# Performance work log

Measured on AMD Instinct MI355X. Metric: run time of the kernel, lower is better.

Reference implementation:

```python
import jax, jax.numpy as jnp
import numpy as np

EMBED_DIM = 512
SE_HIDDEN = max(1, int(EMBED_DIM * 0.25))  # 128
LN_EPS = 1e-5


def setup_inputs() -> dict:
    key = jax.random.key(0)
    ks = jax.random.split(key, 16)
    B, H, W, D = 8, 32, 32, EMBED_DIM
    s = 0.02
    return {
        "q": jax.random.normal(ks[0], (B, H, W, D), jnp.float32),
        "k": jax.random.normal(ks[1], (B, H, W, D), jnp.float32),
        "v": jax.random.normal(ks[2], (B, H, W, D), jnp.float32),
        # Linear weights stored as [in, out] (equivalent to torch W.T)
        "Wq": jax.random.normal(ks[3], (D, D), jnp.float32) * s,
        "Wk": jax.random.normal(ks[4], (D, D), jnp.float32) * s,
        "Wv": jax.random.normal(ks[5], (D, D), jnp.float32) * s,
        "Wo": jax.random.normal(ks[6], (D, D), jnp.float32) * s,
        # Conv2d kernel in HWIO layout for NHWC conv
        "conv_w": jax.random.normal(ks[7], (3, 3, D, D), jnp.float32) * s,
        "conv_b": jnp.zeros((D,), jnp.float32),
        "se_w1": jax.random.normal(ks[8], (D, SE_HIDDEN), jnp.float32) * s,
        "se_b1": jnp.zeros((SE_HIDDEN,), jnp.float32),
        "se_w2": jax.random.normal(ks[9], (SE_HIDDEN, D), jnp.float32) * s,
        "se_b2": jnp.zeros((D,), jnp.float32),
        "ln_g": jnp.ones((D,), jnp.float32),
        "ln_b": jnp.zeros((D,), jnp.float32),
    }


def _layernorm(x, g, b):
    mu = jnp.mean(x, axis=-1, keepdims=True)
    var = jnp.mean(jnp.square(x - mu), axis=-1, keepdims=True)
    return (x - mu) * jax.lax.rsqrt(var + LN_EPS) * g + b


def reference(q, k, v, Wq, Wk, Wv, Wo, conv_w, conv_b,
              se_w1, se_b1, se_w2, se_b2, ln_g, ln_b):
    B, H, W, D = q.shape
    scaler = jnp.sqrt(jnp.asarray(D, q.dtype))
    qp = q @ Wq  # [B,H,W,D]
    kp = k @ Wk
    vp = v @ Wv
    N = H * W
    qf = qp.reshape(B, N, D)
    kf = kp.reshape(B, N, D)
    vf = vp.reshape(B, N, D)
    scores = jnp.einsum('bnd,bmd->bnm', qf, kf) / scaler
    probs = jax.nn.softmax(scores, axis=-1)  # dropout p=0 -> identity
    out = jnp.einsum('bnm,bmd->bnd', probs, vf).reshape(B, H, W, D)
    out = out @ Wo
    # 3x3 same conv in NHWC
    out = jax.lax.conv_general_dilated(
        out, conv_w, window_strides=(1, 1), padding='SAME',
        dimension_numbers=('NHWC', 'HWIO', 'NHWC')) + conv_b
    # squeeze-excite: global average pool over spatial dims
    se = jnp.mean(out, axis=(1, 2))  # [B,D]
    se = jax.nn.silu(se @ se_w1 + se_b1)
    se = jax.nn.sigmoid(se @ se_w2 + se_b2)  # [B,D]
    out = out * se[:, None, None, :]
    x = qp + out  # residual uses q AFTER q_proj (q reassigned in torch code)
    return _layernorm(x, ln_g, ln_b)
```

## Files before the change

kernel.cpp:

```cpp
#include <hip/hip_runtime.h>
#include <hip/hip_bf16.h>

using bf16 = __hip_bfloat16;
typedef __attribute__((ext_vector_type(8))) short short8;
typedef __attribute__((ext_vector_type(4))) float f32x4;

static const size_t OFF_QP   = 0;
static const size_t OFF_KP   = (size_t)8  << 20;
static const size_t OFF_VPT  = (size_t)16 << 20;
static const size_t OFF_SC   = (size_t)24 << 20;
static const size_t OFF_PA   = (size_t)40 << 20;
static const size_t OFF_WT   = (size_t)56 << 20;
static const size_t OFF_CWT  = (size_t)58 << 20;
static const size_t OFF_POOL = (size_t)63 << 20;
static const size_t OFF_SE   = ((size_t)63 << 20) + 16384;
static const size_t OFF_RS   = ((size_t)63 << 20) + 32768;

__global__ __launch_bounds__(256) void prep_k(const float* __restrict__ Wq,
                                              const float* __restrict__ Wk,
                                              const float* __restrict__ Wv,
                                              const float* __restrict__ Wo,
                                              const float* __restrict__ convw,
                                              bf16* __restrict__ wT,
                                              bf16* __restrict__ cwT,
                                              float* __restrict__ pooled) {
    long idx = (long)blockIdx.x * 256 + threadIdx.x;
    if (idx < 4l * 262144) {
        int m = (int)(idx >> 18);
        int o = (int)(idx & 262143);
        int n = o >> 9, k = o & 511;
        const float* W = (m == 0) ? Wq : (m == 1) ? Wk : (m == 2) ? Wv : Wo;
        wT[idx] = __float2bfloat16(W[k * 512 + n]);
    } else if (idx < 4l * 262144 + 512l * 4608) {
        long o = idx - 4l * 262144;
        int co = (int)(o / 4608), t = (int)(o % 4608);
        cwT[o] = __float2bfloat16(convw[(long)t * 512 + co]);
    } else if (idx < 4l * 262144 + 512l * 4608 + 4096) {
        pooled[idx - (4l * 262144 + 512l * 4608)] = 0.f;
    }
}

__device__ __forceinline__ float bf2f(unsigned short h) {
    union { unsigned int u; float f; } c;
    c.u = (unsigned int)h << 16;
    return c.f;
}

template <int OP>
__global__ __launch_bounds__(256, 2) void gemm_k(
    const void* __restrict__ Ap0, const void* __restrict__ Ap1, const void* __restrict__ Ap2,
    int lda, long sA,
    const bf16* __restrict__ BT, int ldb, long sB,
    void* __restrict__ Cp, int ldc, long sC,
    int K, const float* __restrict__ bias, float* __restrict__ pooled,
    float* __restrict__ rs) {
    __shared__ bf16 As[2][128 * 64];
    __shared__ bf16 Bs[2][128 * 64];
    const int tid = threadIdx.x;
    const int l = tid & 63, w = tid >> 6;
    const int wm = w >> 1, wn = w & 1;

    const int gx = gridDim.x, gy = gridDim.y;
    const int nwg = gx * gy * gridDim.z;
    const int bid = blockIdx.x + gx * (blockIdx.y + gy * blockIdx.z);
    const int swz = (bid & 7) * (nwg >> 3) + (bid >> 3);
    const int bx = swz % gx;
    const int rem = swz / gx;
    const int by = rem % gy;
    const int zb = rem / gy;

    const int m0 = by * 128, n0 = bx * 128;
    const float isc = 0.04419417382415922f;

    int kbase = 0;
    const bf16* Ab = nullptr;
    const float* Af = nullptr;
    const bf16* Bb = BT;
    if (OP == 1) {
        Af = (const float*)(zb == 0 ? Ap0 : zb == 1 ? Ap1 : Ap2);
        Bb = BT + (long)zb * 262144;
    } else if (OP == 2) {
        Ab = (const bf16*)Ap0 + (long)zb * sA;
        Bb = BT + (long)zb * sB;
    } else if (OP == 3) {
        Ab = (const bf16*)Ap0;
        kbase = zb * 2304;
    } else if (OP == 4) {
        Ab = (const bf16*)Ap0 + (long)(zb & 7) * sA;
        Bb = BT + (long)(zb & 7) * sB;
        kbase = (zb >> 3) * 512;
    } else {
        Ab = (const bf16*)Ap0;
    }

    const int fr = l & 15;
    f32x4 acc[4][4] = {};
    float esum[4] = {0.f, 0.f, 0.f, 0.f};

    int pixoff[4], hh_[4], wp_[4];
    if (OP == 3) {
#pragma unroll
        for (int i = 0; i < 4; ++i) {
            int s = tid + i * 256;
            int row = s >> 3, c = s & 7;
            int p = m0 + row;
            int bb = p >> 10;
            hh_[i] = (p >> 5) & 31;
            wp_[i] = p & 31;
            pixoff[i] = ((bb * 32 + hh_[i]) * 32 + wp_[i]) * 512 + c * 8;
        }
    }
    float rinv_[4];
    if (OP == 5) {
#pragma unroll
        for (int i = 0; i < 4; ++i) {
            int row = m0 + ((tid + i * 256) >> 3);
            rinv_[i] = 1.0f / (rs[row] + rs[8192 + row]);
        }
    }

    short8 ar[4];
    float4 af0[4], af1[4];
    short8 br[4];

    auto stage_load = [&](int t) {
        int k0 = kbase + t * 64;
        int dy = 0, dx = 0, doff = 0;
        if (OP == 3) {
            int tap = k0 >> 9;
            dy = tap / 3 - 1;
            dx = tap % 3 - 1;
            doff = (dy * 32 + dx) * 512 + (k0 & 511);
        }
#pragma unroll
        for (int i = 0; i < 4; ++i) {
            int s = tid + i * 256;
            int row = s >> 3, c = s & 7;
            if (OP == 1) {
                const float* src = Af + (long)(m0 + row) * lda + k0 + c * 8;
                af0[i] = *(const float4*)src;
                af1[i] = *(const float4*)(src + 4);
            } else if (OP == 3) {
                int h2 = hh_[i] + dy, w2 = wp_[i] + dx;
                if (((unsigned)h2 < 32u) & ((unsigned)w2 < 32u)) {
                    ar[i] = *(const short8*)(Ab + pixoff[i] + doff);
                } else {
                    short8 zz = {0, 0, 0, 0, 0, 0, 0, 0};
                    ar[i] = zz;
                }
            } else if (OP == 4) {
                union { short8 s8; unsigned short h[8]; } u, o;
                u.s8 = *(const short8*)(Ab + (long)(m0 + row) * lda + k0 + c * 8);
                float es = 0.f;
#pragma unroll
                for (int j = 0; j < 8; ++j) {
                    float e = __expf(bf2f(u.h[j]));
                    es += e;
                    union { float f; unsigned int ui; } cf;
                    cf.f = e;
                    o.h[j] = (unsigned short)(cf.ui >> 16);
                }
                esum[i] += es;
                ar[i] = o.s8;
            } else if (OP == 5) {
                union { short8 s8; unsigned short h[8]; } u0, u1, o;
                long off = (long)(m0 + row) * lda + k0 + c * 8;
                u0.s8 = *(const short8*)(Ab + off);
                u1.s8 = *(const short8*)(Ab + 4194304 + off);
#pragma unroll
                for (int j = 0; j < 8; ++j) {
                    bf16 b = __float2bfloat16((bf2f(u0.h[j]) + bf2f(u1.h[j])) * rinv_[i]);
                    o.h[j] = *(unsigned short*)&b;
                }
                ar[i] = o.s8;
            } else {
                ar[i] = *(const short8*)(Ab + (long)(m0 + row) * lda + k0 + c * 8);
            }
        }
#pragma unroll
        for (int i = 0; i < 4; ++i) {
            int s = tid + i * 256;
            int row = s >> 3, c = s & 7;
            br[i] = *(const short8*)(Bb + (long)(n0 + row) * ldb + k0 + c * 8);
        }
    };

    auto stage_write = [&](int b) {
#pragma unroll
        for (int i = 0; i < 4; ++i) {
            int s = tid + i * 256;
            int row = s >> 3, c = s & 7;
            int cx = c ^ (row & 7);
            if (OP == 1) {
                union { short8 s8; bf16 h[8]; } u;
                u.h[0] = __float2bfloat16(af0[i].x); u.h[1] = __float2bfloat16(af0[i].y);
                u.h[2] = __float2bfloat16(af0[i].z); u.h[3] = __float2bfloat16(af0[i].w);
                u.h[4] = __float2bfloat16(af1[i].x); u.h[5] = __float2bfloat16(af1[i].y);
                u.h[6] = __float2bfloat16(af1[i].z); u.h[7] = __float2bfloat16(af1[i].w);
                *(short8*)(&As[b][row * 64 + cx * 8]) = u.s8;
            } else {
                *(short8*)(&As[b][row * 64 + cx * 8]) = ar[i];
            }
        }
#pragma unroll
        for (int i = 0; i < 4; ++i) {
            int s = tid + i * 256;
            int row = s >> 3, c = s & 7;
            int cx = c ^ (row & 7);
            *(short8*)(&Bs[b][row * 64 + cx * 8]) = br[i];
        }
    };

    auto compute = [&](int b) {
#pragma unroll
        for (int h = 0; h < 2; ++h) {
            int cx = ((l >> 4) + 4 * h) ^ (fr & 7);
            short8 afr[4], bfv[4];
#pragma unroll
            for (int m = 0; m < 4; ++m) {
                int r = wm * 64 + m * 16 + fr;
                afr[m] = *(const short8*)(&As[b][r * 64 + cx * 8]);
            }
#pragma unroll
            for (int n = 0; n < 4; ++n) {
                int r = wn * 64 + n * 16 + fr;
                bfv[n] = *(const short8*)(&Bs[b][r * 64 + cx * 8]);
            }
#pragma unroll
            for (int m = 0; m < 4; ++m)
#pragma unroll
                for (int n = 0; n < 4; ++n)
                    acc[m][n] = __builtin_amdgcn_mfma_f32_16x16x32_bf16(afr[m], bfv[n], acc[m][n], 0, 0, 0);
        }
    };

    const int nt = K >> 6;
    stage_load(0);
    stage_write(0);
    int cur = 0;
    for (int t = 0; t < nt; ++t) {
        __syncthreads();
        if (t + 1 < nt) stage_load(t + 1);
        compute(cur);
        if (t + 1 < nt) stage_write(cur ^ 1);
        cur ^= 1;
    }

    if (OP == 4) {
        __syncthreads();
        float* fl = (float*)&As[0][0];
#pragma unroll
        for (int i = 0; i < 4; ++i) {
            int s = tid + i * 256;
            fl[(s >> 3) * 8 + (s & 7)] = esum[i];
        }
        __syncthreads();
        if (bx == 0 && tid < 128) {
            float s8 = 0.f;
#pragma unroll
            for (int j = 0; j < 8; ++j) s8 += fl[tid * 8 + j];
            rs[(zb >> 3) * 8192 + (zb & 7) * 1024 + m0 + tid] = s8;
        }
    }

    const int cr = (l >> 4) * 4, cc = l & 15;
    float csum[4] = {0.f, 0.f, 0.f, 0.f};
#pragma unroll
    for (int m = 0; m < 4; ++m) {
#pragma unroll
        for (int n = 0; n < 4; ++n) {
#pragma unroll
            for (int j = 0; j < 4; ++j) {
                int r = m0 + wm * 64 + m * 16 + cr + j;
                int c = n0 + wn * 64 + n * 16 + cc;
                float vv = acc[m][n][j];
                if (OP == 3) {
                    if (zb == 0) vv += bias[c];
                    csum[n] += vv;
                    ((bf16*)Cp)[(long)zb * 4194304 + (long)r * ldc + c] = __float2bfloat16(vv);
                } else if (OP == 2) {
                    ((bf16*)Cp)[(long)zb * sC + (long)r * ldc + c] = __float2bfloat16(vv);
                } else if (OP == 4) {
                    ((bf16*)Cp)[(long)(zb >> 3) * 4194304 +
                                ((long)(zb & 7) * 1024 + r) * 512 + c] = __float2bfloat16(vv);
                } else if (OP == 5) {
                    ((bf16*)Cp)[(long)r * ldc + c] = __float2bfloat16(vv);
                } else {
                    if (zb == 2) {
                        ((bf16*)Cp)[(size_t)(OFF_VPT / 2) + ((long)(r >> 10) * 512 + c) * 1024 + (r & 1023)] =
                            __float2bfloat16(vv);
                    } else {
                        float sv = (zb == 1) ? vv * isc : vv;
                        ((bf16*)Cp)[(long)zb * 4194304 + (long)r * 512 + c] = __float2bfloat16(sv);
                    }
                }
            }
        }
    }
    if (OP == 3) {
        int bb = m0 >> 10;
#pragma unroll
        for (int n = 0; n < 4; ++n) {
            int c = n0 + wn * 64 + n * 16 + cc;
            atomicAdd(&pooled[bb * 512 + c], csum[n] * (1.0f / 1024.0f));
        }
    }
}

__global__ __launch_bounds__(512) void se_mlp_k(const float* __restrict__ pooled,
                                                const float* __restrict__ w1,
                                                const float* __restrict__ b1,
                                                const float* __restrict__ w2,
                                                const float* __restrict__ b2,
                                                float* __restrict__ se) {
    __shared__ float pl[512];
    __shared__ float part[4][128];
    __shared__ float hid[128];
    const int b = blockIdx.x, t = threadIdx.x;
    pl[t] = pooled[b * 512 + t];
    __syncthreads();
    const int j = t & 127, r = t >> 7;
    float acc = 0.f;
#pragma unroll 8
    for (int s = 0; s < 128; ++s) {
        int i = r * 128 + s;
        acc += pl[i] * w1[i * 128 + j];
    }
    part[r][j] = acc;
    __syncthreads();
    if (t < 128) {
        float a = part[0][t] + part[1][t] + part[2][t] + part[3][t] + b1[t];
        hid[t] = a / (1.f + __expf(-a));
    }
    __syncthreads();
    float acc2 = b2[t];
#pragma unroll 8
    for (int jj = 0; jj < 128; ++jj)
        acc2 += hid[jj] * w2[jj * 512 + t];
    se[b * 512 + t] = 1.f / (1.f + __expf(-acc2));
}

__global__ __launch_bounds__(256) void final_k(const bf16* __restrict__ Pc,
                                               const float* __restrict__ se,
                                               const bf16* __restrict__ qp,
                                               const float* __restrict__ g,
                                               const float* __restrict__ bta,
                                               float* __restrict__ out) {
    __shared__ float red[256];
    long p = blockIdx.x;
    int b = (int)(p >> 10);
    int t = threadIdx.x;
    float x[2];
#pragma unroll
    for (int i = 0; i < 2; ++i) {
        int c = t + i * 256;
        float cv = __bfloat162float(Pc[p * 512 + c]) +
                   __bfloat162float(Pc[4194304 + p * 512 + c]);
        x[i] = __bfloat162float(qp[p * 512 + c]) + cv * se[b * 512 + c];
    }
    red[t] = x[0] + x[1];
    __syncthreads();
    for (int s = 128; s > 0; s >>= 1) {
        if (t < s) red[t] += red[t + s];
        __syncthreads();
    }
    float mu = red[0] * (1.0f / 512.0f);
    __syncthreads();
    float d0 = x[0] - mu, d1 = x[1] - mu;
    red[t] = d0 * d0 + d1 * d1;
    __syncthreads();
    for (int s = 128; s > 0; s >>= 1) {
        if (t < s) red[t] += red[t + s];
        __syncthreads();
    }
    float inv = rsqrtf(red[0] * (1.0f / 512.0f) + 1e-5f);
#pragma unroll
    for (int i = 0; i < 2; ++i) {
        int c = t + i * 256;
        out[p * 512 + c] = (x[i] - mu) * inv * g[c] + bta[c];
    }
}

extern "C" void kernel_launch(void* const* d_in, const int* in_sizes, int n_in,
                              void* d_out, int out_size, void* d_ws, size_t ws_size,
                              hipStream_t stream) {
    const float* q      = (const float*)d_in[0];
    const float* k      = (const float*)d_in[1];
    const float* v      = (const float*)d_in[2];
    const float* Wq     = (const float*)d_in[3];
    const float* Wk     = (const float*)d_in[4];
    const float* Wv     = (const float*)d_in[5];
    const float* Wo     = (const float*)d_in[6];
    const float* convw  = (const float*)d_in[7];
    const float* convb  = (const float*)d_in[8];
    const float* se_w1  = (const float*)d_in[9];
    const float* se_b1  = (const float*)d_in[10];
    const float* se_w2  = (const float*)d_in[11];
    const float* se_b2  = (const float*)d_in[12];
    const float* ln_g   = (const float*)d_in[13];
    const float* ln_b   = (const float*)d_in[14];

    char* ws = (char*)d_ws;
    bf16*  qp     = (bf16*)(ws + OFF_QP);
    bf16*  kp     = (bf16*)(ws + OFF_KP);
    bf16*  vpT    = (bf16*)(ws + OFF_VPT);
    bf16*  out2   = (bf16*)(ws + OFF_VPT);
    bf16*  scores = (bf16*)(ws + OFF_SC);
    bf16*  Pattn  = (bf16*)(ws + OFF_PA);
    bf16*  Pconv  = (bf16*)(ws + OFF_SC);
    bf16*  wT     = (bf16*)(ws + OFF_WT);
    bf16*  cwT    = (bf16*)(ws + OFF_CWT);
    float* pooled = (float*)(ws + OFF_POOL);
    float* se     = (float*)(ws + OFF_SE);
    float* rsums  = (float*)(ws + OFF_RS);

    prep_k<<<13328, 256, 0, stream>>>(Wq, Wk, Wv, Wo, convw, wT, cwT, pooled);

    gemm_k<1><<<dim3(4, 64, 3), 256, 0, stream>>>(q, k, v, 512, 0, wT, 512, 0,
                                                  ws, 512, 0, 512, nullptr, nullptr, nullptr);
    gemm_k<2><<<dim3(8, 8, 8), 256, 0, stream>>>(qp, nullptr, nullptr, 512, 1024l * 512,
                                                 kp, 512, 1024l * 512,
                                                 scores, 1024, 1024l * 1024, 512, nullptr, nullptr, nullptr);
    gemm_k<4><<<dim3(4, 8, 16), 256, 0, stream>>>(scores, nullptr, nullptr, 1024, 1024l * 1024,
                                                  vpT, 1024, 512l * 1024,
                                                  Pattn, 512, 0, 512, nullptr, nullptr, rsums);
    gemm_k<5><<<dim3(4, 64, 1), 256, 0, stream>>>(Pattn, nullptr, nullptr, 512, 0,
                                                  wT + 3 * 262144, 512, 0,
                                                  out2, 512, 0, 512, nullptr, nullptr, rsums);
    gemm_k<3><<<dim3(4, 64, 2), 256, 0, stream>>>(out2, nullptr, nullptr, 0, 0,
                                                  cwT, 4608, 0,
                                                  Pconv, 512, 0, 2304, convb, pooled, nullptr);
    se_mlp_k<<<8, 512, 0, stream>>>(pooled, se_w1, se_b1, se_w2, se_b2, se);
    final_k<<<8192, 256, 0, stream>>>(Pconv, se, qp, ln_g, ln_b, (float*)d_out);
}
```

Baseline: 198.9 us.

## Split conv into dedicated kernel with 4-way split-K and higher occupancy

Moves the 3x3 conv implicit GEMM out of the generic gemm template into its own kernel. The new kernel uses a 32-wide K tile with swizzled shared-memory layout, half the LDS, and a 4-blocks-per-CU launch bound. It also raises split-K from 2 to 4, giving 1024 workgroups instead of 512, to fill the GPU better. The cost is two extra bf16 partial buffers that must be written and then summed in the final LayerNorm kernel, which adds memory traffic and another bf16 rounding step.

```diff
diff --git a/kernel.cpp b/kernel.cpp
--- a/kernel.cpp
+++ b/kernel.cpp
@@ -52,8 +52,7 @@
     int lda, long sA,
     const bf16* __restrict__ BT, int ldb, long sB,
     void* __restrict__ Cp, int ldc, long sC,
-    int K, const float* __restrict__ bias, float* __restrict__ pooled,
-    float* __restrict__ rs) {
+    int K, float* __restrict__ rs) {
     __shared__ bf16 As[2][128 * 64];
     __shared__ bf16 Bs[2][128 * 64];
     const int tid = threadIdx.x;
@@ -82,9 +81,6 @@
     } else if (OP == 2) {
         Ab = (const bf16*)Ap0 + (long)zb * sA;
         Bb = BT + (long)zb * sB;
-    } else if (OP == 3) {
-        Ab = (const bf16*)Ap0;
-        kbase = zb * 2304;
     } else if (OP == 4) {
         Ab = (const bf16*)Ap0 + (long)(zb & 7) * sA;
         Bb = BT + (long)(zb & 7) * sB;
@@ -97,19 +93,6 @@
     f32x4 acc[4][4] = {};
     float esum[4] = {0.f, 0.f, 0.f, 0.f};
 
-    int pixoff[4], hh_[4], wp_[4];
-    if (OP == 3) {
-#pragma unroll
-        for (int i = 0; i < 4; ++i) {
-            int s = tid + i * 256;
-            int row = s >> 3, c = s & 7;
-            int p = m0 + row;
-            int bb = p >> 10;
-            hh_[i] = (p >> 5) & 31;
-            wp_[i] = p & 31;
-            pixoff[i] = ((bb * 32 + hh_[i]) * 32 + wp_[i]) * 512 + c * 8;
-        }
-    }
     float rinv_[4];
     if (OP == 5) {
 #pragma unroll
@@ -125,13 +108,6 @@
 
     auto stage_load = [&](int t) {
         int k0 = kbase + t * 64;
-        int dy = 0, dx = 0, doff = 0;
-        if (OP == 3) {
-            int tap = k0 >> 9;
-            dy = tap / 3 - 1;
-            dx = tap % 3 - 1;
-            doff = (dy * 32 + dx) * 512 + (k0 & 511);
-        }
 #pragma unroll
         for (int i = 0; i < 4; ++i) {
             int s = tid + i * 256;
@@ -140,14 +116,6 @@
                 const float* src = Af + (long)(m0 + row) * lda + k0 + c * 8;
                 af0[i] = *(const float4*)src;
                 af1[i] = *(const float4*)(src + 4);
-            } else if (OP == 3) {
-                int h2 = hh_[i] + dy, w2 = wp_[i] + dx;
-                if (((unsigned)h2 < 32u) & ((unsigned)w2 < 32u)) {
-                    ar[i] = *(const short8*)(Ab + pixoff[i] + doff);
-                } else {
-                    short8 zz = {0, 0, 0, 0, 0, 0, 0, 0};
-                    ar[i] = zz;
-                }
             } else if (OP == 4) {
                 union { short8 s8; unsigned short h[8]; } u, o;
                 u.s8 = *(const short8*)(Ab + (long)(m0 + row) * lda + k0 + c * 8);
@@ -264,7 +232,6 @@
     }
 
     const int cr = (l >> 4) * 4, cc = l & 15;
-    float csum[4] = {0.f, 0.f, 0.f, 0.f};
 #pragma unroll
     for (int m = 0; m < 4; ++m) {
 #pragma unroll
@@ -274,11 +241,7 @@
                 int r = m0 + wm * 64 + m * 16 + cr + j;
                 int c = n0 + wn * 64 + n * 16 + cc;
                 float vv = acc[m][n][j];
-                if (OP == 3) {
-                    if (zb == 0) vv += bias[c];
-                    csum[n] += vv;
-                    ((bf16*)Cp)[(long)zb * 4194304 + (long)r * ldc + c] = __float2bfloat16(vv);
-                } else if (OP == 2) {
+                if (OP == 2) {
                     ((bf16*)Cp)[(long)zb * sC + (long)r * ldc + c] = __float2bfloat16(vv);
                 } else if (OP == 4) {
                     ((bf16*)Cp)[(long)(zb >> 3) * 4194304 +
@@ -297,13 +260,142 @@
             }
         }
     }
-    if (OP == 3) {
-        int bb = m0 >> 10;
+}
+
+__global__ __launch_bounds__(256, 4) void conv_k(
+    const bf16* __restrict__ A,
+    const bf16* __restrict__ BT,
+    bf16* __restrict__ P,
+    const float* __restrict__ bias,
+    float* __restrict__ pooled) {
+    __shared__ bf16 As[2][128 * 32];
+    __shared__ bf16 Bs[2][128 * 32];
+    const int tid = threadIdx.x;
+    const int l = tid & 63, w = tid >> 6;
+    const int wm = w >> 1, wn = w & 1;
+
+    const int gx = 4, gy = 64, nwg = 1024;
+    const int bid = blockIdx.x + gx * (blockIdx.y + gy * blockIdx.z);
+    const int swz = (bid & 7) * (nwg >> 3) + (bid >> 3);
+    const int bx = swz % gx;
+    const int rem = swz / gx;
+    const int by = rem % gy;
+    const int zb = rem / gy;
+
+    const int m0 = by * 128, n0 = bx * 128;
+    const int kbase = zb * 1152;
+
+    const int fr = l & 15;
+    const int ck = (l >> 4) ^ ((fr >> 1) & 3);
+    f32x4 acc[4][4] = {};
+
+    int pixoff[2], hh_[2], wp_[2];
+#pragma unroll
+    for (int i = 0; i < 2; ++i) {
+        int s = tid + i * 256;
+        int row = s >> 2, c = s & 3;
+        int p = m0 + row;
+        int bb = p >> 10;
+        hh_[i] = (p >> 5) & 31;
+        wp_[i] = p & 31;
+        pixoff[i] = ((bb * 32 + hh_[i]) * 32 + wp_[i]) * 512 + c * 8;
+    }
+
+    short8 ar[2], br[2];
+
+    auto stage_load = [&](int t) {
+        int k0 = kbase + t * 32;
+        int tap = k0 >> 9;
+        int dy = tap / 3 - 1, dx = tap % 3 - 1;
+        int doff = (dy * 32 + dx) * 512 + (k0 & 511);
+#pragma unroll
+        for (int i = 0; i < 2; ++i) {
+            int h2 = hh_[i] + dy, w2 = wp_[i] + dx;
+            if (((unsigned)h2 < 32u) & ((unsigned)w2 < 32u)) {
+                ar[i] = *(const short8*)(A + pixoff[i] + doff);
+            } else {
+                short8 zz = {0, 0, 0, 0, 0, 0, 0, 0};
+                ar[i] = zz;
+            }
+        }
+#pragma unroll
+        for (int i = 0; i < 2; ++i) {
+            int s = tid + i * 256;
+            int row = s >> 2, c = s & 3;
+            br[i] = *(const short8*)(BT + (long)(n0 + row) * 4608 + k0 + c * 8);
+        }
+    };
+
+    auto stage_write = [&](int b) {
+#pragma unroll
+        for (int i = 0; i < 2; ++i) {
+            int s = tid + i * 256;
+            int row = s >> 2, c = s & 3;
+            int c2 = c ^ ((row >> 1) & 3);
+            *(short8*)(&As[b][row * 32 + c2 * 8]) = ar[i];
+        }
+#pragma unroll
+        for (int i = 0; i < 2; ++i) {
+            int s = tid + i * 256;
+            int row = s >> 2, c = s & 3;
+            int c2 = c ^ ((row >> 1) & 3);
+            *(short8*)(&Bs[b][row * 32 + c2 * 8]) = br[i];
+        }
+    };
+
+    auto compute = [&](int b) {
+        short8 af[4], bf[4];
+#pragma unroll
+        for (int m = 0; m < 4; ++m) {
+            int r = wm * 64 + m * 16 + fr;
+            af[m] = *(const short8*)(&As[b][r * 32 + ck * 8]);
+        }
 #pragma unroll
         for (int n = 0; n < 4; ++n) {
-            int c = n0 + wn * 64 + n * 16 + cc;
-            atomicAdd(&pooled[bb * 512 + c], csum[n] * (1.0f / 1024.0f));
-        }
+            int r = wn * 64 + n * 16 + fr;
+            bf[n] = *(const short8*)(&Bs[b][r * 32 + ck * 8]);
+        }
+#pragma unroll
+        for (int m = 0; m < 4; ++m)
+#pragma unroll
+            for (int n = 0; n < 4; ++n)
+                acc[m][n] = __builtin_amdgcn_mfma_f32_16x16x32_bf16(af[m], bf[n], acc[m][n], 0, 0, 0);
+    };
+
+    const int nt = 36;
+    stage_load(0);
+    stage_write(0);
+    int cur = 0;
+    for (int t = 0; t < nt; ++t) {
+        __syncthreads();
+        if (t + 1 < nt) stage_load(t + 1);
+        compute(cur);
+        if (t + 1 < nt) stage_write(cur ^ 1);
+        cur ^= 1;
+    }
+
+    const int cr = (l >> 4) * 4, cc = l & 15;
+    float csum[4] = {0.f, 0.f, 0.f, 0.f};
+#pragma unroll
+    for (int m = 0; m < 4; ++m) {
+#pragma unroll
+        for (int n = 0; n < 4; ++n) {
+#pragma unroll
+            for (int j = 0; j < 4; ++j) {
+                int r = m0 + wm * 64 + m * 16 + cr + j;
+                int c = n0 + wn * 64 + n * 16 + cc;
+                float vv = acc[m][n][j];
+                if (zb == 0) vv += bias[c];
+                csum[n] += vv;
+                P[(long)zb * 4194304 + (long)r * 512 + c] = __float2bfloat16(vv);
+            }
+        }
+    }
+    int bb = m0 >> 10;
+#pragma unroll
+    for (int n = 0; n < 4; ++n) {
+        int c = n0 + wn * 64 + n * 16 + cc;
+        atomicAdd(&pooled[bb * 512 + c], csum[n] * (1.0f / 1024.0f));
     }
 }
 
@@ -354,9 +446,10 @@
 #pragma unroll
     for (int i = 0; i < 2; ++i) {
         int c = t + i * 256;
-        float cv = __bfloat162float(Pc[p * 512 + c]) +
-                   __bfloat162float(Pc[4194304 + p * 512 + c]);
-        x[i] = __bfloat162float(qp[p * 512 + c]) + cv * se[b * 512 + c];
+        long o = p * 512 + c;
+        float cv = __bfloat162float(Pc[o]) + __bfloat162float(Pc[4194304 + o]) +
+                   __bfloat162float(Pc[2l * 4194304 + o]) + __bfloat162float(Pc[3l * 4194304 + o]);
+        x[i] = __bfloat162float(qp[o]) + cv * se[b * 512 + c];
     }
     red[t] = x[0] + x[1];
     __syncthreads();
@@ -417,19 +510,17 @@
     prep_k<<<13328, 256, 0, stream>>>(Wq, Wk, Wv, Wo, convw, wT, cwT, pooled);
 
     gemm_k<1><<<dim3(4, 64, 3), 256, 0, stream>>>(q, k, v, 512, 0, wT, 512, 0,
-                                                  ws, 512, 0, 512, nullptr, nullptr, nullptr);
+                                                  ws, 512, 0, 512, nullptr);
     gemm_k<2><<<dim3(8, 8, 8), 256, 0, stream>>>(qp, nullptr, nullptr, 512, 1024l * 512,
                                                  kp, 512, 1024l * 512,
-                                                 scores, 1024, 1024l * 1024, 512, nullptr, nullptr, nullptr);
+                                                 scores, 1024, 1024l * 1024, 512, nullptr);
     gemm_k<4><<<dim3(4, 8, 16), 256, 0, stream>>>(scores, nullptr, nullptr, 1024, 1024l * 1024,
                                                   vpT, 1024, 512l * 1024,
-                                                  Pattn, 512, 0, 512, nullptr, nullptr, rsums);
+                                                  Pattn, 512, 0, 512, rsums);
     gemm_k<5><<<dim3(4, 64, 1), 256, 0, stream>>>(Pattn, nullptr, nullptr, 512, 0,
                                                   wT + 3 * 262144, 512, 0,
-                                                  out2, 512, 0, 512, nullptr, nullptr, rsums);
-    gemm_k<3><<<dim3(4, 64, 2), 256, 0, stream>>>(out2, nullptr, nullptr, 0, 0,
-                                                  cwT, 4608, 0,
-                                                  Pconv, 512, 0, 2304, convb, pooled, nullptr);
+                                                  out2, 512, 0, 512, rsums);
+    conv_k<<<dim3(4, 64, 4), 256, 0, stream>>>(out2, cwT, Pconv, convb, pooled);
     se_mlp_k<<<8, 512, 0, stream>>>(pooled, se_w1, se_b1, se_w2, se_b2, se);
     final_k<<<8192, 256, 0, stream>>>(Pconv, se, qp, ln_g, ln_b, (float*)d_out);
 }
```

New measurement: 221.7 us. 1.11x slower.
